# Optimization experiments

Measured on AMD Instinct MI355X. Metric: run time of the kernel, lower is better.

The kernel has to match this reference:

```python
import jax, jax.numpy as jnp
import numpy as np

DIM = 1024
HEADS = 16
HEAD_DIM = DIM // HEADS
FF_MULT = 2
ROPE_BASE = 10000.0
EPS = 1e-6
B, S = 2, 2048


def setup_inputs() -> dict:
    key = jax.random.key(0)
    ks = jax.random.split(key, 6)
    sc = lambda fan_in: 1.0 / np.sqrt(fan_in)
    return {
        "x": jax.random.normal(ks[0], (B, S, DIM), dtype=jnp.float32),
        "w_in_norm": jnp.ones((DIM,), dtype=jnp.float32),
        "w_ff_norm": jnp.ones((DIM,), dtype=jnp.float32),
        "w_qkv": jax.random.normal(ks[1], (3 * DIM, DIM), dtype=jnp.float32) * sc(DIM),
        "w_out": jax.random.normal(ks[2], (DIM, DIM), dtype=jnp.float32) * sc(DIM),
        "w_fc": jax.random.normal(ks[3], (DIM * FF_MULT, DIM), dtype=jnp.float32) * sc(DIM),
        "w_proj": jax.random.normal(ks[4], (DIM, DIM * FF_MULT), dtype=jnp.float32) * sc(DIM * FF_MULT),
    }


def rmsnorm(x, w):
    var = jnp.mean(jnp.square(x), axis=-1, keepdims=True)
    return x * jax.lax.rsqrt(var + EPS) * w


def rope_tables(seq_len):
    half = HEAD_DIM // 2
    inv_freq = 1.0 / (ROPE_BASE ** (2.0 * jnp.arange(half, dtype=jnp.float32) / HEAD_DIM))
    angles = jnp.arange(seq_len, dtype=jnp.float32)[:, None] * inv_freq[None, :]  # (S, half)
    return jnp.cos(angles), jnp.sin(angles)


def apply_rope(x, cos, sin):
    # x: (B, H, S, D); interleaved pairs along last dim
    xp = x.reshape(*x.shape[:-1], HEAD_DIM // 2, 2)
    x_even, x_odd = xp[..., 0], xp[..., 1]
    c = cos.astype(x.dtype)  # (S, half) broadcasts over (B, H)
    s = sin.astype(x.dtype)
    rot_even = x_even * c - x_odd * s
    rot_odd = x_odd * c + x_even * s
    return jnp.stack([rot_even, rot_odd], axis=-1).reshape(x.shape)


def reference(x, w_in_norm, w_ff_norm, w_qkv, w_out, w_fc, w_proj):
    b, s, d = x.shape
    # --- attention sub-block (pre-norm) ---
    h = rmsnorm(x, w_in_norm)
    qkv = jnp.einsum("bsd,ed->bse", h, w_qkv)  # (B, S, 3*D)
    q, k, v = jnp.split(qkv, 3, axis=-1)
    def heads(t):
        return t.reshape(b, s, HEADS, HEAD_DIM).transpose(0, 2, 1, 3)  # (B, H, S, Dh)
    q, k, v = heads(q), heads(k), heads(v)
    cos, sin = rope_tables(s)
    q = apply_rope(q, cos, sin)
    k = apply_rope(k, cos, sin)
    scale = 1.0 / np.sqrt(HEAD_DIM)
    scores = jnp.einsum("bhqd,bhkd->bhqk", q, k) * scale
    causal = jnp.tril(jnp.ones((s, s), dtype=bool))
    scores = jnp.where(causal, scores, jnp.finfo(scores.dtype).min)
    probs = jax.nn.softmax(scores, axis=-1)
    attn = jnp.einsum("bhqk,bhkd->bhqd", probs, v)
    attn = attn.transpose(0, 2, 1, 3).reshape(b, s, d)
    x = x + jnp.einsum("bsd,ed->bse", attn, w_out)
    # --- feed-forward sub-block (pre-norm) ---
    h = rmsnorm(x, w_ff_norm)
    hid = jax.nn.silu(jnp.einsum("bsd,fd->bsf", h, w_fc))
    x = x + jnp.einsum("bsf,df->bsd", hid, w_proj)
    return x
```

## Files before the change

kernel.cpp:

```cpp
#include <hip/hip_runtime.h>
#include <hip/hip_bf16.h>
#include <cstdint>

#define DIMSZ 1024
#define S_LEN 2048
#define NH 16
#define HD 64

typedef __attribute__((ext_vector_type(4))) float f32x4;
typedef __attribute__((ext_vector_type(8))) __bf16 bf16x8;

#define MFMA_BF16(a,b,c) __builtin_amdgcn_mfma_f32_16x16x32_bf16((a),(b),(c),0,0,0)

__device__ __forceinline__ void gload_lds16(const void* g, void* l) {
  __builtin_amdgcn_global_load_lds(
      (const __attribute__((address_space(1))) unsigned int*)(uintptr_t)g,
      (__attribute__((address_space(3))) unsigned int*)(uintptr_t)l,
      16, 0, 0);
}

__global__ __launch_bounds__(256)
void cast_all_kernel(const float* __restrict__ s0, const float* __restrict__ s1,
                     const float* __restrict__ s2, const float* __restrict__ s3,
                     __hip_bfloat16* __restrict__ d0, __hip_bfloat16* __restrict__ d1,
                     __hip_bfloat16* __restrict__ d2, __hip_bfloat16* __restrict__ d3)
{
  int i = blockIdx.x * 256 + threadIdx.x;
  const float* s; __hip_bfloat16* d; int off;
  if (i < 786432)       { s = s0; d = d0; off = i; }
  else if (i < 1048576) { s = s1; d = d1; off = i - 786432; }
  else if (i < 1572864) { s = s2; d = d2; off = i - 1048576; }
  else                  { s = s3; d = d3; off = i - 1572864; }
  float4 v = ((const float4*)s)[off];
  __hip_bfloat16* o = d + (size_t)off * 4;
  o[0] = __float2bfloat16(v.x);
  o[1] = __float2bfloat16(v.y);
  o[2] = __float2bfloat16(v.z);
  o[3] = __float2bfloat16(v.w);
}

__global__ __launch_bounds__(256)
void rmsnorm_kernel(const float* __restrict__ x, const float* __restrict__ w,
                    __hip_bfloat16* __restrict__ out)
{
  int row = blockIdx.x;
  int tid = threadIdx.x;
  const float4 v = ((const float4*)(x + (size_t)row * DIMSZ))[tid];
  float ss = v.x*v.x + v.y*v.y + v.z*v.z + v.w*v.w;
  #pragma unroll
  for (int m = 32; m >= 1; m >>= 1) ss += __shfl_xor(ss, m);
  __shared__ float red[4];
  int wave = tid >> 6, lane = tid & 63;
  if (lane == 0) red[wave] = ss;
  __syncthreads();
  float tot = red[0] + red[1] + red[2] + red[3];
  float sc = rsqrtf(tot * (1.0f / DIMSZ) + 1e-6f);
  const float4 wv = ((const float4*)w)[tid];
  __hip_bfloat16* o = out + (size_t)row * DIMSZ + tid * 4;
  o[0] = __float2bfloat16(v.x * sc * wv.x);
  o[1] = __float2bfloat16(v.y * sc * wv.y);
  o[2] = __float2bfloat16(v.z * sc * wv.z);
  o[3] = __float2bfloat16(v.w * sc * wv.w);
}

template<int EPI>
__global__ __launch_bounds__(256, 2)
void gemm_bt2(const __hip_bfloat16* __restrict__ A,
              const __hip_bfloat16* __restrict__ Bw,
              float* __restrict__ Cf,
              __hip_bfloat16* __restrict__ Cb,
              const float* __restrict__ resid,
              int N, int K)
{
  __shared__ __align__(16) char sA[2][16384];
  __shared__ __align__(16) char sB[2][16384];
  const int tid = threadIdx.x;
  const int wave = tid >> 6, lane = tid & 63;
  const int lg = lane >> 4, lr15 = lane & 15;
  const int row0 = blockIdx.y * 128, col0 = blockIdx.x * 128;
  const int wr = wave >> 1, wc = wave & 1;
  f32x4 acc[4][4] = {};

  const size_t Kb = (size_t)K * 2;
  const int rown = tid >> 3;
  const int scol = ((tid & 7) << 4) ^ ((rown & 7) << 4);
  const char* gA = (const char*)A + (size_t)(row0 + rown) * Kb + scol;
  const char* gB = (const char*)Bw + (size_t)(col0 + rown) * Kb + scol;
  const int dbase = wave * 1024;

  const int nsteps = K >> 6;
  int cur = 0;

#define STAGE_G(buf, st) do {                                              \
    const size_t kb_ = (size_t)(st) * 128;                                 \
    _Pragma("unroll")                                                      \
    for (int it = 0; it < 4; ++it) {                                       \
      gload_lds16(gA + (size_t)(it * 32) * Kb + kb_, &sA[buf][it * 4096 + dbase]); \
      gload_lds16(gB + (size_t)(it * 32) * Kb + kb_, &sB[buf][it * 4096 + dbase]); \
    }                                                                      \
  } while (0)

  STAGE_G(0, 0);
  __syncthreads();

  const int swz = (lr15 & 7) << 4;
  for (int st = 0; st < nsteps; ++st) {
    if (st + 1 < nsteps) STAGE_G(cur ^ 1, st + 1);
    const char* pA = sA[cur];
    const char* pB = sB[cur];
    bf16x8 af[2][4], bfr[2][4];
    #pragma unroll
    for (int m = 0; m < 4; ++m) {
      const int ra = (wr * 64 + m * 16 + lr15) * 128;
      af[0][m] = *(const bf16x8*)(pA + ra + ((lg * 16) ^ swz));
      af[1][m] = *(const bf16x8*)(pA + ra + ((64 + lg * 16) ^ swz));
      const int rb = (wc * 64 + m * 16 + lr15) * 128;
      bfr[0][m] = *(const bf16x8*)(pB + rb + ((lg * 16) ^ swz));
      bfr[1][m] = *(const bf16x8*)(pB + rb + ((64 + lg * 16) ^ swz));
    }
    #pragma unroll
    for (int kh = 0; kh < 2; ++kh)
      #pragma unroll
      for (int m = 0; m < 4; ++m)
        #pragma unroll
        for (int n = 0; n < 4; ++n)
          acc[m][n] = MFMA_BF16(af[kh][m], bfr[kh][n], acc[m][n]);
    __syncthreads();
    cur ^= 1;
  }
#undef STAGE_G

  #pragma unroll
  for (int m = 0; m < 4; ++m) {
    #pragma unroll
    for (int n = 0; n < 4; ++n) {
      #pragma unroll
      for (int r = 0; r < 4; ++r) {
        const int grow = row0 + wr * 64 + m * 16 + lg * 4 + r;
        const int gcol = col0 + wc * 64 + n * 16 + lr15;
        const size_t idx = (size_t)grow * N + gcol;
        const float v = acc[m][n][r];
        if (EPI == 0) {
          Cb[idx] = __float2bfloat16(v);
        } else if (EPI == 1) {
          Cf[idx] = resid[idx] + v;
        } else {
          Cb[idx] = __float2bfloat16(v / (1.0f + __expf(-v)));
        }
      }
    }
  }
}

__global__ __launch_bounds__(256)
void rope_qk(const __hip_bfloat16* __restrict__ qkv,
             __hip_bfloat16* __restrict__ Q, __hip_bfloat16* __restrict__ Kx)
{
  int idx = blockIdx.x * 256 + threadIdx.x;
  int i = idx & 31;
  int h = (idx >> 5) & 15;
  int s = (idx >> 9) & (S_LEN - 1);
  int b = idx >> 20;
  const size_t base = ((size_t)b * S_LEN + s) * 3072 + h * 64 + 2 * i;
  float qe = __bfloat162float(qkv[base]);
  float qo = __bfloat162float(qkv[base + 1]);
  float ke = __bfloat162float(qkv[base + 1024]);
  float ko = __bfloat162float(qkv[base + 1025]);
  float inv = __expf(-(2.0f * i) * (9.210340371976184f / 64.0f));
  float ang = (float)s * inv;
  float sn, cs;
  __sincosf(ang, &sn, &cs);
  const float sc = 0.125f;
  size_t qb = (((size_t)b * NH + h) * S_LEN + s) * HD + 2 * i;
  Q[qb]     = __float2bfloat16((qe * cs - qo * sn) * sc);
  Q[qb + 1] = __float2bfloat16((qo * cs + qe * sn) * sc);
  Kx[qb]     = __float2bfloat16(ke * cs - ko * sn);
  Kx[qb + 1] = __float2bfloat16(ko * cs + ke * sn);
}

__global__ __launch_bounds__(256)
void v_transpose(const __hip_bfloat16* __restrict__ qkv, __hip_bfloat16* __restrict__ Vt)
{
  __shared__ __hip_bfloat16 t[64][72];
  const int s0 = blockIdx.x * 64;
  const int bh = blockIdx.y;
  const int b = bh >> 4, h = bh & 15;
  const int tid = threadIdx.x;
  const int c = tid & 63;
  #pragma unroll
  for (int r = 0; r < 16; ++r) {
    int srow = r * 4 + (tid >> 6);
    t[srow][c] = qkv[((size_t)b * S_LEN + s0 + srow) * 3072 + 2048 + h * 64 + c];
  }
  __syncthreads();
  #pragma unroll
  for (int r = 0; r < 16; ++r) {
    int drow = r * 4 + (tid >> 6);
    Vt[(((size_t)b * NH + h) * HD + drow) * S_LEN + s0 + c] = t[c][drow];
  }
}

__device__ __forceinline__ unsigned bf16pack2(float a, float b) {
  __hip_bfloat16 ha = __float2bfloat16(a), hb = __float2bfloat16(b);
  unsigned ua = *reinterpret_cast<unsigned short*>(&ha);
  unsigned ub = *reinterpret_cast<unsigned short*>(&hb);
  return ua | (ub << 16);
}

__global__ __launch_bounds__(512, 4)
void flash_attn4(const __hip_bfloat16* __restrict__ Q,
                 const __hip_bfloat16* __restrict__ Kx,
                 const __hip_bfloat16* __restrict__ Vt,
                 __hip_bfloat16* __restrict__ attn)
{
  __shared__ __align__(16) char sK[2][8192];
  __shared__ __align__(16) char sV[2][8192];
  __shared__ __align__(16) char sP[8][2048];

  const int tid = threadIdx.x;
  const int w = tid >> 6;
  const int lane = tid & 63;
  const int lg = lane >> 4, lr = lane & 15;
  const int bid = blockIdx.x;
  const int bh = bid & 31;
  const int b = bh >> 4, h = bh & 15;
  const int u = (bid >> 5) & 7;
  const int rnd = bid >> 8;
  const int qb = rnd == 0 ? (u << 1) : (15 - (u << 1));
  const int q0 = qb << 7;
  const int nsteps = (qb << 1) + 2;

  const char* Kb = (const char*)(Kx + (size_t)bh * S_LEN * HD);
  const char* Vb = (const char*)(Vt + (size_t)bh * HD * S_LEN);
  const __hip_bfloat16* Qp = Q + (size_t)bh * S_LEN * HD;

  const int q0w = q0 + w * 16;
  const bf16x8 qf0 = *(const bf16x8*)&Qp[(q0w + lr) * HD + lg * 8];
  const bf16x8 qf1 = *(const bf16x8*)&Qp[(q0w + lr) * HD + 32 + lg * 8];
  char* sPw = sP[w];
  const int swzr = (lr & 7) << 4;
  const int srow = tid >> 3;
  const int scol = ((tid & 7) << 4) ^ ((srow & 7) << 4);
  const int wbase = w << 10;

  f32x4 acc[4] = {};
  float lsum = 0.f;
  int cur = 0;

  gload_lds16(Kb + (size_t)srow * 128 + scol, sK[0] + wbase);
  gload_lds16(Vb + (size_t)srow * (S_LEN * 2) + scol, sV[0] + wbase);
  __syncthreads();

  for (int st = 0; st < nsteps; ++st) {
    if (st + 1 < nsteps) {
      const size_t kn = (size_t)(st + 1) * 64;
      gload_lds16(Kb + (kn + srow) * 128 + scol, sK[cur ^ 1] + wbase);
      gload_lds16(Vb + (size_t)srow * (S_LEN * 2) + kn * 2 + scol, sV[cur ^ 1] + wbase);
    }
    const int k0 = st * 64;
    const char* pK = sK[cur];
    const char* pV = sV[cur];
    f32x4 sv[4];
    __builtin_amdgcn_s_setprio(1);
    #pragma unroll
    for (int t = 0; t < 4; ++t) {
      const int rb = (t * 16 + lr) * 128;
      const bf16x8 kf0 = *(const bf16x8*)(pK + rb + ((lg * 16) ^ swzr));
      const bf16x8 kf1 = *(const bf16x8*)(pK + rb + ((64 + lg * 16) ^ swzr));
      f32x4 z = {};
      z = MFMA_BF16(kf0, qf0, z);
      z = MFMA_BF16(kf1, qf1, z);
      sv[t] = z;
    }
    __builtin_amdgcn_s_setprio(0);
    const bool maskstep = (st >= nsteps - 2);
    #pragma unroll
    for (int t = 0; t < 4; ++t) {
      float p[4];
      #pragma unroll
      for (int r = 0; r < 4; ++r) {
        float e = __expf(sv[t][r]);
        if (maskstep) {
          const int kg = k0 + t * 16 + lg * 4 + r;
          e = (kg <= q0w + lr) ? e : 0.f;
        }
        lsum += e;
        p[r] = e;
      }
      uint2 wv2;
      wv2.x = bf16pack2(p[0], p[1]);
      wv2.y = bf16pack2(p[2], p[3]);
      *(uint2*)(sPw + lr * 128 + ((t * 32 + lg * 8) ^ swzr)) = wv2;
    }
    asm volatile("s_waitcnt lgkmcnt(0)" ::: "memory");
    __builtin_amdgcn_sched_barrier(0);
    const bf16x8 pa0 = *(const bf16x8*)(sPw + lr * 128 + ((lg * 16) ^ swzr));
    const bf16x8 pa1 = *(const bf16x8*)(sPw + lr * 128 + ((64 + lg * 16) ^ swzr));
    __builtin_amdgcn_s_setprio(1);
    #pragma unroll
    for (int dt = 0; dt < 4; ++dt) {
      const int rb = (dt * 16 + lr) * 128;
      const bf16x8 vf0 = *(const bf16x8*)(pV + rb + ((lg * 16) ^ swzr));
      const bf16x8 vf1 = *(const bf16x8*)(pV + rb + ((64 + lg * 16) ^ swzr));
      acc[dt] = MFMA_BF16(pa0, vf0, acc[dt]);
      acc[dt] = MFMA_BF16(pa1, vf1, acc[dt]);
    }
    __builtin_amdgcn_s_setprio(0);
    __syncthreads();
    cur ^= 1;
  }

  lsum += __shfl_xor(lsum, 16);
  lsum += __shfl_xor(lsum, 32);
  #pragma unroll
  for (int r = 0; r < 4; ++r) {
    const float li = __shfl(lsum, lg * 4 + r);
    const float rli = 1.0f / li;
    const size_t rowb = ((size_t)b * S_LEN + q0w + lg * 4 + r) * DIMSZ + h * HD;
    #pragma unroll
    for (int dt = 0; dt < 4; ++dt)
      attn[rowb + dt * 16 + lr] = __float2bfloat16(acc[dt][r] * rli);
  }
}

extern "C" void kernel_launch(void* const* d_in, const int* in_sizes, int n_in,
                              void* d_out, int out_size, void* d_ws, size_t ws_size,
                              hipStream_t stream)
{
  const float* x      = (const float*)d_in[0];
  const float* w_in   = (const float*)d_in[1];
  const float* w_ff   = (const float*)d_in[2];
  const float* w_qkv  = (const float*)d_in[3];
  const float* w_out  = (const float*)d_in[4];
  const float* w_fc   = (const float*)d_in[5];
  const float* w_proj = (const float*)d_in[6];
  float* out = (float*)d_out;
  char* ws = (char*)d_ws;

  __hip_bfloat16* wq_b   = (__hip_bfloat16*)(ws);
  __hip_bfloat16* wo_b   = (__hip_bfloat16*)(ws + 6291456);
  __hip_bfloat16* wfc_b  = (__hip_bfloat16*)(ws + 8388608);
  __hip_bfloat16* wpr_b  = (__hip_bfloat16*)(ws + 12582912);
  __hip_bfloat16* h_b    = (__hip_bfloat16*)(ws + 16777216);
  __hip_bfloat16* qkv_b  = (__hip_bfloat16*)(ws + 25165824);
  __hip_bfloat16* attn_b = (__hip_bfloat16*)(ws + 25165824);
  __hip_bfloat16* hid_b  = (__hip_bfloat16*)(ws + 33554432);
  __hip_bfloat16* Q_b    = (__hip_bfloat16*)(ws + 50331648);
  __hip_bfloat16* K_b    = (__hip_bfloat16*)(ws + 58720256);
  __hip_bfloat16* Vt_b   = (__hip_bfloat16*)(ws + 67108864);
  float*          x1     = (float*)(ws + 50331648);

  cast_all_kernel<<<8192, 256, 0, stream>>>(w_qkv, w_out, w_fc, w_proj, wq_b, wo_b, wfc_b, wpr_b);
  rmsnorm_kernel<<<4096, 256, 0, stream>>>(x, w_in, h_b);
  gemm_bt2<0><<<dim3(3072 / 128, 4096 / 128), 256, 0, stream>>>(h_b, wq_b, nullptr, qkv_b, nullptr, 3072, 1024);
  rope_qk<<<2097152 / 256, 256, 0, stream>>>(qkv_b, Q_b, K_b);
  v_transpose<<<dim3(32, 32), 256, 0, stream>>>(qkv_b, Vt_b);
  flash_attn4<<<512, 512, 0, stream>>>(Q_b, K_b, Vt_b, attn_b);
  gemm_bt2<1><<<dim3(1024 / 128, 4096 / 128), 256, 0, stream>>>(attn_b, wo_b, x1, nullptr, x, 1024, 1024);
  rmsnorm_kernel<<<4096, 256, 0, stream>>>(x1, w_ff, h_b);
  gemm_bt2<2><<<dim3(2048 / 128, 4096 / 128), 256, 0, stream>>>(h_b, wfc_b, nullptr, hid_b, nullptr, 2048, 1024);
  gemm_bt2<1><<<dim3(1024 / 128, 4096 / 128), 256, 0, stream>>>(hid_b, wpr_b, out, nullptr, x1, 1024, 2048);
}
```

Before: 173.9 us.

## Single-buffer GEMM LDS for higher occupancy and fold log2e into Q scale

Measured after the change: 193.2 us. 1.11x slower.

```diff
diff --git a/kernel.cpp b/kernel.cpp
--- a/kernel.cpp
+++ b/kernel.cpp
@@ -1,6 +1,7 @@
 #include <hip/hip_runtime.h>
 #include <hip/hip_bf16.h>
 #include <cstdint>
+#include <cmath>
 
 #define DIMSZ 1024
 #define S_LEN 2048
@@ -64,16 +65,16 @@
 }
 
 template<int EPI>
-__global__ __launch_bounds__(256, 2)
-void gemm_bt2(const __hip_bfloat16* __restrict__ A,
+__global__ __launch_bounds__(256, 4)
+void gemm_bt3(const __hip_bfloat16* __restrict__ A,
               const __hip_bfloat16* __restrict__ Bw,
               float* __restrict__ Cf,
               __hip_bfloat16* __restrict__ Cb,
               const float* __restrict__ resid,
               int N, int K)
 {
-  __shared__ __align__(16) char sA[2][16384];
-  __shared__ __align__(16) char sB[2][16384];
+  __shared__ __align__(16) char sA[16384];
+  __shared__ __align__(16) char sB[16384];
   const int tid = threadIdx.x;
   const int wave = tid >> 6, lane = tid & 63;
   const int lg = lane >> 4, lr15 = lane & 15;
@@ -89,34 +90,25 @@
   const int dbase = wave * 1024;
 
   const int nsteps = K >> 6;
-  int cur = 0;
-
-#define STAGE_G(buf, st) do {                                              \
-    const size_t kb_ = (size_t)(st) * 128;                                 \
-    _Pragma("unroll")                                                      \
-    for (int it = 0; it < 4; ++it) {                                       \
-      gload_lds16(gA + (size_t)(it * 32) * Kb + kb_, &sA[buf][it * 4096 + dbase]); \
-      gload_lds16(gB + (size_t)(it * 32) * Kb + kb_, &sB[buf][it * 4096 + dbase]); \
-    }                                                                      \
-  } while (0)
-
-  STAGE_G(0, 0);
-  __syncthreads();
-
   const int swz = (lr15 & 7) << 4;
+
   for (int st = 0; st < nsteps; ++st) {
-    if (st + 1 < nsteps) STAGE_G(cur ^ 1, st + 1);
-    const char* pA = sA[cur];
-    const char* pB = sB[cur];
+    const size_t kb_ = (size_t)st * 128;
+    #pragma unroll
+    for (int it = 0; it < 4; ++it) {
+      gload_lds16(gA + (size_t)(it * 32) * Kb + kb_, &sA[it * 4096 + dbase]);
+      gload_lds16(gB + (size_t)(it * 32) * Kb + kb_, &sB[it * 4096 + dbase]);
+    }
+    __syncthreads();
     bf16x8 af[2][4], bfr[2][4];
     #pragma unroll
     for (int m = 0; m < 4; ++m) {
       const int ra = (wr * 64 + m * 16 + lr15) * 128;
-      af[0][m] = *(const bf16x8*)(pA + ra + ((lg * 16) ^ swz));
-      af[1][m] = *(const bf16x8*)(pA + ra + ((64 + lg * 16) ^ swz));
+      af[0][m] = *(const bf16x8*)(sA + ra + ((lg * 16) ^ swz));
+      af[1][m] = *(const bf16x8*)(sA + ra + ((64 + lg * 16) ^ swz));
       const int rb = (wc * 64 + m * 16 + lr15) * 128;
-      bfr[0][m] = *(const bf16x8*)(pB + rb + ((lg * 16) ^ swz));
-      bfr[1][m] = *(const bf16x8*)(pB + rb + ((64 + lg * 16) ^ swz));
+      bfr[0][m] = *(const bf16x8*)(sB + rb + ((lg * 16) ^ swz));
+      bfr[1][m] = *(const bf16x8*)(sB + rb + ((64 + lg * 16) ^ swz));
     }
     #pragma unroll
     for (int kh = 0; kh < 2; ++kh)
@@ -126,9 +118,7 @@
         for (int n = 0; n < 4; ++n)
           acc[m][n] = MFMA_BF16(af[kh][m], bfr[kh][n], acc[m][n]);
     __syncthreads();
-    cur ^= 1;
-  }
-#undef STAGE_G
+  }
 
   #pragma unroll
   for (int m = 0; m < 4; ++m) {
@@ -170,7 +160,7 @@
   float ang = (float)s * inv;
   float sn, cs;
   __sincosf(ang, &sn, &cs);
-  const float sc = 0.125f;
+  const float sc = 0.125f * 1.4426950408889634f;
   size_t qb = (((size_t)b * NH + h) * S_LEN + s) * HD + 2 * i;
   Q[qb]     = __float2bfloat16((qe * cs - qo * sn) * sc);
   Q[qb + 1] = __float2bfloat16((qo * cs + qe * sn) * sc);
@@ -208,7 +198,7 @@
 }
 
 __global__ __launch_bounds__(512, 4)
-void flash_attn4(const __hip_bfloat16* __restrict__ Q,
+void flash_attn6(const __hip_bfloat16* __restrict__ Q,
                  const __hip_bfloat16* __restrict__ Kx,
                  const __hip_bfloat16* __restrict__ Vt,
                  __hip_bfloat16* __restrict__ attn)
@@ -279,7 +269,7 @@
       float p[4];
       #pragma unroll
       for (int r = 0; r < 4; ++r) {
-        float e = __expf(sv[t][r]);
+        float e = exp2f(sv[t][r]);
         if (maskstep) {
           const int kg = k0 + t * 16 + lg * 4 + r;
           e = (kg <= q0w + lr) ? e : 0.f;
@@ -352,12 +342,12 @@
 
   cast_all_kernel<<<8192, 256, 0, stream>>>(w_qkv, w_out, w_fc, w_proj, wq_b, wo_b, wfc_b, wpr_b);
   rmsnorm_kernel<<<4096, 256, 0, stream>>>(x, w_in, h_b);
-  gemm_bt2<0><<<dim3(3072 / 128, 4096 / 128), 256, 0, stream>>>(h_b, wq_b, nullptr, qkv_b, nullptr, 3072, 1024);
+  gemm_bt3<0><<<dim3(3072 / 128, 4096 / 128), 256, 0, stream>>>(h_b, wq_b, nullptr, qkv_b, nullptr, 3072, 1024);
   rope_qk<<<2097152 / 256, 256, 0, stream>>>(qkv_b, Q_b, K_b);
   v_transpose<<<dim3(32, 32), 256, 0, stream>>>(qkv_b, Vt_b);
-  flash_attn4<<<512, 512, 0, stream>>>(Q_b, K_b, Vt_b, attn_b);
-  gemm_bt2<1><<<dim3(1024 / 128, 4096 / 128), 256, 0, stream>>>(attn_b, wo_b, x1, nullptr, x, 1024, 1024);
+  flash_attn6<<<512, 512, 0, stream>>>(Q_b, K_b, Vt_b, attn_b);
+  gemm_bt3<1><<<dim3(1024 / 128, 4096 / 128), 256, 0, stream>>>(attn_b, wo_b, x1, nullptr, x, 1024, 1024);
   rmsnorm_kernel<<<4096, 256, 0, stream>>>(x1, w_ff, h_b);
-  gemm_bt2<2><<<dim3(2048 / 128, 4096 / 128), 256, 0, stream>>>(h_b, wfc_b, nullptr, hid_b, nullptr, 2048, 1024);
-  gemm_bt2<1><<<dim3(1024 / 128, 4096 / 128), 256, 0, stream>>>(hid_b, wpr_b, out, nullptr, x1, 1024, 2048);
-}
+  gemm_bt3<2><<<dim3(2048 / 128, 4096 / 128), 256, 0, stream>>>(h_b, wfc_b, nullptr, hid_b, nullptr, 2048, 1024);
+  gemm_bt3<1><<<dim3(1024 / 128, 4096 / 128), 256, 0, stream>>>(hid_b, wpr_b, out, nullptr, x1, 1024, 2048);
+}
```

## Merge prep and rope/transpose launches, store residual stream x1 in bf16

Applied to the files above, without the earlier changes.

Result: faster. 169.5 us (-2.5%).

```diff
diff --git a/kernel.cpp b/kernel.cpp
--- a/kernel.cpp
+++ b/kernel.cpp
@@ -19,34 +19,64 @@
       16, 0, 0);
 }
 
+__device__ __forceinline__ float bf16bits2f(unsigned short u) {
+  return __uint_as_float((unsigned)u << 16);
+}
+
 __global__ __launch_bounds__(256)
-void cast_all_kernel(const float* __restrict__ s0, const float* __restrict__ s1,
-                     const float* __restrict__ s2, const float* __restrict__ s3,
-                     __hip_bfloat16* __restrict__ d0, __hip_bfloat16* __restrict__ d1,
-                     __hip_bfloat16* __restrict__ d2, __hip_bfloat16* __restrict__ d3)
-{
-  int i = blockIdx.x * 256 + threadIdx.x;
-  const float* s; __hip_bfloat16* d; int off;
-  if (i < 786432)       { s = s0; d = d0; off = i; }
-  else if (i < 1048576) { s = s1; d = d1; off = i - 786432; }
-  else if (i < 1572864) { s = s2; d = d2; off = i - 1048576; }
-  else                  { s = s3; d = d3; off = i - 1572864; }
-  float4 v = ((const float4*)s)[off];
-  __hip_bfloat16* o = d + (size_t)off * 4;
-  o[0] = __float2bfloat16(v.x);
-  o[1] = __float2bfloat16(v.y);
-  o[2] = __float2bfloat16(v.z);
-  o[3] = __float2bfloat16(v.w);
+void prep_kernel(const float* __restrict__ s0, const float* __restrict__ s1,
+                 const float* __restrict__ s2, const float* __restrict__ s3,
+                 __hip_bfloat16* __restrict__ d0, __hip_bfloat16* __restrict__ d1,
+                 __hip_bfloat16* __restrict__ d2, __hip_bfloat16* __restrict__ d3,
+                 const float* __restrict__ x, const float* __restrict__ w_in,
+                 __hip_bfloat16* __restrict__ h)
+{
+  __shared__ float red[4];
+  const int bid = blockIdx.x;
+  const int tid = threadIdx.x;
+  if (bid < 8192) {
+    int i = bid * 256 + tid;
+    const float* s; __hip_bfloat16* d; int off;
+    if (i < 786432)       { s = s0; d = d0; off = i; }
+    else if (i < 1048576) { s = s1; d = d1; off = i - 786432; }
+    else if (i < 1572864) { s = s2; d = d2; off = i - 1048576; }
+    else                  { s = s3; d = d3; off = i - 1572864; }
+    float4 v = ((const float4*)s)[off];
+    __hip_bfloat16* o = d + (size_t)off * 4;
+    o[0] = __float2bfloat16(v.x);
+    o[1] = __float2bfloat16(v.y);
+    o[2] = __float2bfloat16(v.z);
+    o[3] = __float2bfloat16(v.w);
+    return;
+  }
+  const int row = bid - 8192;
+  const float4 v = ((const float4*)(x + (size_t)row * DIMSZ))[tid];
+  float ss = v.x*v.x + v.y*v.y + v.z*v.z + v.w*v.w;
+  #pragma unroll
+  for (int m = 32; m >= 1; m >>= 1) ss += __shfl_xor(ss, m);
+  int wave = tid >> 6, lane = tid & 63;
+  if (lane == 0) red[wave] = ss;
+  __syncthreads();
+  float tot = red[0] + red[1] + red[2] + red[3];
+  float sc = rsqrtf(tot * (1.0f / DIMSZ) + 1e-6f);
+  const float4 wv = ((const float4*)w_in)[tid];
+  __hip_bfloat16* o = h + (size_t)row * DIMSZ + tid * 4;
+  o[0] = __float2bfloat16(v.x * sc * wv.x);
+  o[1] = __float2bfloat16(v.y * sc * wv.y);
+  o[2] = __float2bfloat16(v.z * sc * wv.z);
+  o[3] = __float2bfloat16(v.w * sc * wv.w);
 }
 
 __global__ __launch_bounds__(256)
-void rmsnorm_kernel(const float* __restrict__ x, const float* __restrict__ w,
-                    __hip_bfloat16* __restrict__ out)
+void rmsnorm_bf16_kernel(const __hip_bfloat16* __restrict__ x, const float* __restrict__ w,
+                         __hip_bfloat16* __restrict__ out)
 {
   int row = blockIdx.x;
   int tid = threadIdx.x;
-  const float4 v = ((const float4*)(x + (size_t)row * DIMSZ))[tid];
-  float ss = v.x*v.x + v.y*v.y + v.z*v.z + v.w*v.w;
+  const ushort4 raw = ((const ushort4*)(x + (size_t)row * DIMSZ))[tid];
+  float v0 = bf16bits2f(raw.x), v1 = bf16bits2f(raw.y);
+  float v2 = bf16bits2f(raw.z), v3 = bf16bits2f(raw.w);
+  float ss = v0*v0 + v1*v1 + v2*v2 + v3*v3;
   #pragma unroll
   for (int m = 32; m >= 1; m >>= 1) ss += __shfl_xor(ss, m);
   __shared__ float red[4];
@@ -57,10 +87,10 @@
   float sc = rsqrtf(tot * (1.0f / DIMSZ) + 1e-6f);
   const float4 wv = ((const float4*)w)[tid];
   __hip_bfloat16* o = out + (size_t)row * DIMSZ + tid * 4;
-  o[0] = __float2bfloat16(v.x * sc * wv.x);
-  o[1] = __float2bfloat16(v.y * sc * wv.y);
-  o[2] = __float2bfloat16(v.z * sc * wv.z);
-  o[3] = __float2bfloat16(v.w * sc * wv.w);
+  o[0] = __float2bfloat16(v0 * sc * wv.x);
+  o[1] = __float2bfloat16(v1 * sc * wv.y);
+  o[2] = __float2bfloat16(v2 * sc * wv.z);
+  o[3] = __float2bfloat16(v3 * sc * wv.w);
 }
 
 template<int EPI>
@@ -69,7 +99,8 @@
               const __hip_bfloat16* __restrict__ Bw,
               float* __restrict__ Cf,
               __hip_bfloat16* __restrict__ Cb,
-              const float* __restrict__ resid,
+              const float* __restrict__ residf,
+              const __hip_bfloat16* __restrict__ residb,
               int N, int K)
 {
   __shared__ __align__(16) char sA[2][16384];
@@ -143,9 +174,11 @@
         if (EPI == 0) {
           Cb[idx] = __float2bfloat16(v);
         } else if (EPI == 1) {
-          Cf[idx] = resid[idx] + v;
+          Cb[idx] = __float2bfloat16(residf[idx] + v);
+        } else if (EPI == 2) {
+          Cb[idx] = __float2bfloat16(v / (1.0f + __expf(-v)));
         } else {
-          Cb[idx] = __float2bfloat16(v / (1.0f + __expf(-v)));
+          Cf[idx] = __bfloat162float(residb[idx]) + v;
         }
       }
     }
@@ -153,39 +186,40 @@
 }
 
 __global__ __launch_bounds__(256)
-void rope_qk(const __hip_bfloat16* __restrict__ qkv,
-             __hip_bfloat16* __restrict__ Q, __hip_bfloat16* __restrict__ Kx)
-{
-  int idx = blockIdx.x * 256 + threadIdx.x;
-  int i = idx & 31;
-  int h = (idx >> 5) & 15;
-  int s = (idx >> 9) & (S_LEN - 1);
-  int b = idx >> 20;
-  const size_t base = ((size_t)b * S_LEN + s) * 3072 + h * 64 + 2 * i;
-  float qe = __bfloat162float(qkv[base]);
-  float qo = __bfloat162float(qkv[base + 1]);
-  float ke = __bfloat162float(qkv[base + 1024]);
-  float ko = __bfloat162float(qkv[base + 1025]);
-  float inv = __expf(-(2.0f * i) * (9.210340371976184f / 64.0f));
-  float ang = (float)s * inv;
-  float sn, cs;
-  __sincosf(ang, &sn, &cs);
-  const float sc = 0.125f;
-  size_t qb = (((size_t)b * NH + h) * S_LEN + s) * HD + 2 * i;
-  Q[qb]     = __float2bfloat16((qe * cs - qo * sn) * sc);
-  Q[qb + 1] = __float2bfloat16((qo * cs + qe * sn) * sc);
-  Kx[qb]     = __float2bfloat16(ke * cs - ko * sn);
-  Kx[qb + 1] = __float2bfloat16(ko * cs + ke * sn);
-}
-
-__global__ __launch_bounds__(256)
-void v_transpose(const __hip_bfloat16* __restrict__ qkv, __hip_bfloat16* __restrict__ Vt)
+void rope_vt_kernel(const __hip_bfloat16* __restrict__ qkv,
+                    __hip_bfloat16* __restrict__ Q, __hip_bfloat16* __restrict__ Kx,
+                    __hip_bfloat16* __restrict__ Vt)
 {
   __shared__ __hip_bfloat16 t[64][72];
-  const int s0 = blockIdx.x * 64;
-  const int bh = blockIdx.y;
+  const int bid = blockIdx.x;
+  const int tid = threadIdx.x;
+  if (bid < 8192) {
+    int idx = bid * 256 + tid;
+    int i = idx & 31;
+    int h = (idx >> 5) & 15;
+    int s = (idx >> 9) & (S_LEN - 1);
+    int b = idx >> 20;
+    const size_t base = ((size_t)b * S_LEN + s) * 3072 + h * 64 + 2 * i;
+    float qe = __bfloat162float(qkv[base]);
+    float qo = __bfloat162float(qkv[base + 1]);
+    float ke = __bfloat162float(qkv[base + 1024]);
+    float ko = __bfloat162float(qkv[base + 1025]);
+    float inv = __expf(-(2.0f * i) * (9.210340371976184f / 64.0f));
+    float ang = (float)s * inv;
+    float sn, cs;
+    __sincosf(ang, &sn, &cs);
+    const float sc = 0.125f;
+    size_t qb = (((size_t)b * NH + h) * S_LEN + s) * HD + 2 * i;
+    Q[qb]     = __float2bfloat16((qe * cs - qo * sn) * sc);
+    Q[qb + 1] = __float2bfloat16((qo * cs + qe * sn) * sc);
+    Kx[qb]     = __float2bfloat16(ke * cs - ko * sn);
+    Kx[qb + 1] = __float2bfloat16(ko * cs + ke * sn);
+    return;
+  }
+  const int v = bid - 8192;
+  const int bh = v >> 5;
+  const int s0 = (v & 31) * 64;
   const int b = bh >> 4, h = bh & 15;
-  const int tid = threadIdx.x;
   const int c = tid & 63;
   #pragma unroll
   for (int r = 0; r < 16; ++r) {
@@ -348,16 +382,15 @@
   __hip_bfloat16* Q_b    = (__hip_bfloat16*)(ws + 50331648);
   __hip_bfloat16* K_b    = (__hip_bfloat16*)(ws + 58720256);
   __hip_bfloat16* Vt_b   = (__hip_bfloat16*)(ws + 67108864);
-  float*          x1     = (float*)(ws + 50331648);
-
-  cast_all_kernel<<<8192, 256, 0, stream>>>(w_qkv, w_out, w_fc, w_proj, wq_b, wo_b, wfc_b, wpr_b);
-  rmsnorm_kernel<<<4096, 256, 0, stream>>>(x, w_in, h_b);
-  gemm_bt2<0><<<dim3(3072 / 128, 4096 / 128), 256, 0, stream>>>(h_b, wq_b, nullptr, qkv_b, nullptr, 3072, 1024);
-  rope_qk<<<2097152 / 256, 256, 0, stream>>>(qkv_b, Q_b, K_b);
-  v_transpose<<<dim3(32, 32), 256, 0, stream>>>(qkv_b, Vt_b);
+  __hip_bfloat16* x1b    = (__hip_bfloat16*)(ws + 50331648);
+
+  prep_kernel<<<8192 + 4096, 256, 0, stream>>>(w_qkv, w_out, w_fc, w_proj,
+                                               wq_b, wo_b, wfc_b, wpr_b, x, w_in, h_b);
+  gemm_bt2<0><<<dim3(3072 / 128, 4096 / 128), 256, 0, stream>>>(h_b, wq_b, nullptr, qkv_b, nullptr, nullptr, 3072, 1024);
+  rope_vt_kernel<<<8192 + 1024, 256, 0, stream>>>(qkv_b, Q_b, K_b, Vt_b);
   flash_attn4<<<512, 512, 0, stream>>>(Q_b, K_b, Vt_b, attn_b);
-  gemm_bt2<1><<<dim3(1024 / 128, 4096 / 128), 256, 0, stream>>>(attn_b, wo_b, x1, nullptr, x, 1024, 1024);
-  rmsnorm_kernel<<<4096, 256, 0, stream>>>(x1, w_ff, h_b);
-  gemm_bt2<2><<<dim3(2048 / 128, 4096 / 128), 256, 0, stream>>>(h_b, wfc_b, nullptr, hid_b, nullptr, 2048, 1024);
-  gemm_bt2<1><<<dim3(1024 / 128, 4096 / 128), 256, 0, stream>>>(hid_b, wpr_b, out, nullptr, x1, 1024, 2048);
-}
+  gemm_bt2<1><<<dim3(1024 / 128, 4096 / 128), 256, 0, stream>>>(attn_b, wo_b, nullptr, x1b, x, nullptr, 1024, 1024);
+  rmsnorm_bf16_kernel<<<4096, 256, 0, stream>>>(x1b, w_ff, h_b);
+  gemm_bt2<2><<<dim3(2048 / 128, 4096 / 128), 256, 0, stream>>>(h_b, wfc_b, nullptr, hid_b, nullptr, nullptr, 2048, 1024);
+  gemm_bt2<3><<<dim3(1024 / 128, 4096 / 128), 256, 0, stream>>>(hid_b, wpr_b, out, nullptr, nullptr, x1b, 1024, 2048);
+}
```
